# Performance work log

Hardware: AMD Instinct MI355X
Metric: run time of the kernel (lower is better)

Reference implementation:

```python
import jax, jax.numpy as jnp
import numpy as np

N = 100000
E = 1600000
D_IN, D_HID, D_OUT = 128, 32, 32
NEG_SLOPE = 0.2
EPS = 1e-16


def setup_inputs() -> dict:
    key = jax.random.key(0)
    ks = jax.random.split(key, 9)
    x = jax.random.normal(ks[0], (N, D_IN), dtype=jnp.float32)
    edge_index = jax.random.randint(ks[1], (2, E), 0, N, dtype=jnp.int64)
    W1 = jax.random.normal(ks[2], (D_IN, D_HID), dtype=jnp.float32) / np.sqrt(D_IN)
    b1 = jnp.zeros((D_HID,), dtype=jnp.float32)
    W2 = jax.random.normal(ks[3], (D_HID, D_OUT), dtype=jnp.float32) / np.sqrt(D_HID)
    att_src = jax.random.normal(ks[4], (D_OUT,), dtype=jnp.float32) / np.sqrt(D_OUT)
    att_dst = jax.random.normal(ks[5], (D_OUT,), dtype=jnp.float32) / np.sqrt(D_OUT)
    b2 = jnp.zeros((D_OUT,), dtype=jnp.float32)
    return {"x": x, "edge_index": edge_index, "W1": W1, "b1": b1,
            "W2": W2, "att_src": att_src, "att_dst": att_dst, "b2": b2}


def _add_self_loops(edge_index, n):
    loop = jnp.arange(n, dtype=edge_index.dtype)
    src = jnp.concatenate([edge_index[0], loop])
    dst = jnp.concatenate([edge_index[1], loop])
    return src, dst


def _gcn_conv(x, src, dst, W, b, n):
    # symmetric normalization with self-loops already included
    deg = jax.ops.segment_sum(jnp.ones_like(dst, dtype=x.dtype), dst, num_segments=n)
    dis = jnp.where(deg > 0, jax.lax.rsqrt(jnp.maximum(deg, 1.0)), 0.0)
    h = x @ W                               # [N, H]
    norm = dis[src] * dis[dst]              # [E2]
    msg = norm[:, None] * h[src]            # [E2, H]
    return jax.ops.segment_sum(msg, dst, num_segments=n) + b


def _gat_conv(x, src, dst, W, att_src, att_dst, b, n):
    g = x @ W                               # [N, H]
    a_s = g @ att_src                       # [N]
    a_d = g @ att_dst                       # [N]
    e = a_s[src] + a_d[dst]                 # [E2]
    e = jnp.where(e > 0, e, NEG_SLOPE * e)  # leaky_relu(0.2)
    # segment softmax over edges grouped by destination node
    emax = jax.ops.segment_max(e, dst, num_segments=n)
    ee = jnp.exp(e - emax[dst])
    esum = jax.ops.segment_sum(ee, dst, num_segments=n)
    alpha = ee / (esum[dst] + EPS)
    msg = alpha[:, None] * g[src]           # [E2, H]
    return jax.ops.segment_sum(msg, dst, num_segments=n) + b


def reference(x, edge_index, W1, b1, W2, att_src, att_dst, b2):
    n = x.shape[0]
    src, dst = _add_self_loops(edge_index, n)
    h = _gcn_conv(x, src, dst, W1, b1, n)
    h = jax.nn.relu(h)
    out = _gat_conv(h, src, dst, W2, att_src, att_dst, b2, n)
    return out
```

## Files before the change

### kernel.cpp

```cpp
#include <hip/hip_runtime.h>
#include <cstdint>
#include <cstddef>

#define D_IN   128
#define D_HID  32
#define D_OUT  32
#define NEG_SLOPE 0.2f
#define EPS_F  1e-16f

#define BKT_SHIFT 9
#define NPB (1 << BKT_SHIFT)
#define KBUKMAX 256
#define NBLK_BIN 512
#define AGG_BLOCKS 2048

using half4 = __attribute__((ext_vector_type(4))) _Float16;

__global__ void detect_kernel(const int* __restrict__ ei, long long E, int* __restrict__ flag) {
    const int t = threadIdx.x;
    long long n = E < 64 ? E : 64;
    int bad = (t < n && ei[2 * t + 1] != 0) ? 1 : 0;
    unsigned long long mask = __ballot(bad);
    if (t == 0) *flag = (mask == 0ULL) ? 1 : 0;
}

__device__ __forceinline__ int edge_val(const int* __restrict__ ei, long long idx, int is64) {
    return is64 ? ei[idx * 2] : ei[idx];
}

__global__ __launch_bounds__(256) void hist_kernel(
        const int* __restrict__ ei, const int* __restrict__ flag,
        long long E, long long E2, int* __restrict__ hist, int K2, int EPB) {
    __shared__ int hcnt[KBUKMAX];
    const int is64 = *flag;
    const int t = threadIdx.x;
    if (t < K2) hcnt[t] = 0;
    __syncthreads();
    const long long lo = (long long)blockIdx.x * EPB;
    const long long hi = min(E2, lo + EPB);
    for (long long e = lo + t; e < hi; e += 256) {
        int d = (e < E) ? edge_val(ei, E + e, is64) : (int)(e - E);
        atomicAdd(&hcnt[d >> BKT_SHIFT], 1);
    }
    __syncthreads();
    if (t < K2) hist[t * gridDim.x + blockIdx.x] = hcnt[t];
}

__global__ void scan_ga_kernel(int* __restrict__ a, int* __restrict__ bsum, int L) {
    __shared__ int wsum[4];
    const int t = threadIdx.x;
    const int i0 = blockIdx.x * 1024 + t * 4;
    int v[4]; int s = 0;
    #pragma unroll
    for (int k = 0; k < 4; ++k) {
        v[k] = (i0 + k < L) ? a[i0 + k] : 0;
        s += v[k];
    }
    const int lane = t & 63, wid = t >> 6;
    int incl = s;
    #pragma unroll
    for (int d = 1; d < 64; d <<= 1) {
        int u = __shfl_up(incl, d);
        if (lane >= d) incl += u;
    }
    if (lane == 63) wsum[wid] = incl;
    __syncthreads();
    int woff = 0;
    for (int w = 0; w < wid; ++w) woff += wsum[w];
    int excl = woff + incl - s;
    #pragma unroll
    for (int k = 0; k < 4; ++k) {
        if (i0 + k < L) a[i0 + k] = excl;
        excl += v[k];
    }
    if (t == 255) bsum[blockIdx.x] = woff + incl;
}

__global__ __launch_bounds__(1024) void scan_flat_kernel(int* __restrict__ a, int L) {
    __shared__ int wsum[16];
    __shared__ int carry_s;
    const int t = threadIdx.x;
    const int lane = t & 63, wid = t >> 6;
    if (t == 0) carry_s = 0;
    __syncthreads();
    for (int start = 0; start < L; start += 1024) {
        int idx = start + t;
        int v = (idx < L) ? a[idx] : 0;
        int incl = v;
        #pragma unroll
        for (int d = 1; d < 64; d <<= 1) {
            int u = __shfl_up(incl, d);
            if (lane >= d) incl += u;
        }
        if (lane == 63) wsum[wid] = incl;
        __syncthreads();
        int woff = 0;
        for (int w = 0; w < wid; ++w) woff += wsum[w];
        int carry = carry_s;
        __syncthreads();
        if (idx < L) a[idx] = carry + woff + incl - v;
        if (t == 1023) carry_s = carry + woff + incl;
        __syncthreads();
    }
}

__global__ void scan_gc_kernel(int* __restrict__ a, const int* __restrict__ bsum, int L) {
    int idx = blockIdx.x * blockDim.x + threadIdx.x;
    if (idx < L) a[idx] += bsum[idx >> 10];
}

__global__ __launch_bounds__(256) void scatter_kernel(
        const int* __restrict__ ei, const int* __restrict__ flag,
        long long E, long long E2, const int* __restrict__ off,
        unsigned* __restrict__ bins, int K2, int EPB) {
    __shared__ int cur[KBUKMAX];
    const int is64 = *flag;
    const int t = threadIdx.x;
    if (t < K2) cur[t] = off[t * gridDim.x + blockIdx.x];
    __syncthreads();
    const long long lo = (long long)blockIdx.x * EPB;
    const long long hi = min(E2, lo + EPB);
    for (long long e = lo + t; e < hi; e += 256) {
        int s, d;
        if (e < E) { s = edge_val(ei, e, is64); d = edge_val(ei, E + e, is64); }
        else       { s = d = (int)(e - E); }
        int b = d >> BKT_SHIFT;
        int pos = atomicAdd(&cur[b], 1);
        bins[pos] = (unsigned)s | ((unsigned)(d & (NPB - 1)) << 17);
    }
}

__global__ __launch_bounds__(512) void csr_b_kernel(
        const unsigned* __restrict__ bins, const int* __restrict__ off,
        int* __restrict__ rowptr, float* __restrict__ dis, int* __restrict__ csr_src,
        int N, int K2, long long E2) {
    __shared__ int lcur[NPB];
    __shared__ int wsum[8];
    const int b = blockIdx.x, t = threadIdx.x;
    const int nbase = b << BKT_SHIFT;
    const int nn = min(NPB, N - nbase);
    lcur[t] = 0;
    __syncthreads();
    const int base = off[b * NBLK_BIN];
    const int end  = (b == K2 - 1) ? (int)E2 : off[(b + 1) * NBLK_BIN];
    for (int i = base + t; i < end; i += 512)
        atomicAdd(&lcur[bins[i] >> 17], 1);
    __syncthreads();
    const int lane = t & 63, wid = t >> 6;
    int v = lcur[t];
    int incl = v;
    #pragma unroll
    for (int d = 1; d < 64; d <<= 1) {
        int u = __shfl_up(incl, d);
        if (lane >= d) incl += u;
    }
    if (lane == 63) wsum[wid] = incl;
    __syncthreads();
    int woff = 0;
    for (int w = 0; w < wid; ++w) woff += wsum[w];
    int excl = woff + incl - v;
    if (t < nn) {
        rowptr[nbase + t] = base + excl;
        dis[nbase + t] = rsqrtf((float)v);
    }
    __syncthreads();
    lcur[t] = base + excl;
    __syncthreads();
    for (int i = base + t; i < end; i += 512) {
        unsigned u = bins[i];
        int pos = atomicAdd(&lcur[u >> 17], 1);
        csr_src[pos] = (int)(u & 0x1FFFFu);
    }
    if (b == 0 && t == 0) rowptr[N] = (int)E2;
}

__global__ __launch_bounds__(256) void gemm1_kernel(
        const float* __restrict__ x, const float* __restrict__ W1,
        const float* __restrict__ dis, _Float16* __restrict__ hws_h, int N) {
    __shared__ float sW[D_IN * D_HID];
    const int t = threadIdx.x;
    for (int i = t; i < D_IN * D_HID; i += 256) sW[i] = W1[i];
    __syncthreads();
    long long row = (long long)blockIdx.x * 256 + t;
    const bool valid = row < N;
    long long r = valid ? row : (long long)(N - 1);
    const float4* x4 = (const float4*)x;
    float acc[D_HID];
    #pragma unroll
    for (int c = 0; c < D_HID; ++c) acc[c] = 0.f;
    for (int q = 0; q < 32; ++q) {
        float4 xv = x4[r * 32 + q];
        #pragma unroll
        for (int kk = 0; kk < 4; ++kk) {
            float xs = (&xv.x)[kk];
            const float* wrow = &sW[(q * 4 + kk) * D_HID];
            #pragma unroll
            for (int c4 = 0; c4 < 8; ++c4) {
                float4 wv = *(const float4*)&wrow[c4 * 4];
                acc[c4 * 4 + 0] = fmaf(xs, wv.x, acc[c4 * 4 + 0]);
                acc[c4 * 4 + 1] = fmaf(xs, wv.y, acc[c4 * 4 + 1]);
                acc[c4 * 4 + 2] = fmaf(xs, wv.z, acc[c4 * 4 + 2]);
                acc[c4 * 4 + 3] = fmaf(xs, wv.w, acc[c4 * 4 + 3]);
            }
        }
    }
    if (valid) {
        float dd = dis[r];
        half4* hh4 = (half4*)hws_h;
        #pragma unroll
        for (int c4 = 0; c4 < 8; ++c4) {
            half4 o;
            o.x = (_Float16)(acc[c4 * 4 + 0] * dd);
            o.y = (_Float16)(acc[c4 * 4 + 1] * dd);
            o.z = (_Float16)(acc[c4 * 4 + 2] * dd);
            o.w = (_Float16)(acc[c4 * 4 + 3] * dd);
            hh4[r * 8 + c4] = o;
        }
    }
}

__global__ void gcn_agg_kernel(const int* __restrict__ rowptr, const int* __restrict__ csr_src,
                               const _Float16* __restrict__ hws_h, const float* __restrict__ dis,
                               const float* __restrict__ b1, float* __restrict__ h1, int N) {
    const int lane = threadIdx.x & 63;
    const int u = lane & 7, grp = lane >> 3;
    const int wib = threadIdx.x >> 6;
    const half4* hh4 = (const half4*)hws_h;
    float4* h14 = (float4*)h1;
    const float4 b14 = ((const float4*)b1)[u];
    for (int i = blockIdx.x * 4 + wib; i < N; i += gridDim.x * 4) {
        const int b = rowptr[i], e = rowptr[i + 1];
        float ax = 0.f, ay = 0.f, az = 0.f, aw = 0.f;
        for (int j = b + grp; j < e; j += 8) {
            int s = csr_src[j];
            half4 hv = hh4[s * 8 + u];
            ax += (float)hv.x; ay += (float)hv.y;
            az += (float)hv.z; aw += (float)hv.w;
        }
        #pragma unroll
        for (int d = 8; d <= 32; d <<= 1) {
            ax += __shfl_xor(ax, d); ay += __shfl_xor(ay, d);
            az += __shfl_xor(az, d); aw += __shfl_xor(aw, d);
        }
        if (grp == 0) {
            float dd = dis[i];
            float4 o;
            o.x = fmaf(dd, ax, b14.x); o.y = fmaf(dd, ay, b14.y);
            o.z = fmaf(dd, az, b14.z); o.w = fmaf(dd, aw, b14.w);
            o.x = o.x > 0.f ? o.x : 0.f; o.y = o.y > 0.f ? o.y : 0.f;
            o.z = o.z > 0.f ? o.z : 0.f; o.w = o.w > 0.f ? o.w : 0.f;
            h14[(long long)i * 8 + u] = o;
        }
    }
}

__global__ void gemm2_kernel(const float* __restrict__ h1, const float* __restrict__ W2,
                             const float* __restrict__ att_s, const float* __restrict__ att_d,
                             _Float16* __restrict__ g_h, float* __restrict__ a_s,
                             float* __restrict__ a_d, int N) {
    __shared__ float sW[D_HID * D_OUT];
    __shared__ float sas[D_OUT], sad[D_OUT];
    __shared__ float sh[8][D_HID];
    const int t = threadIdx.x;
    const int c = t & 31, r = t >> 5;
    for (int i = t; i < D_HID * D_OUT; i += 256) sW[i] = W2[i];
    if (t < D_OUT) { sas[t] = att_s[t]; sad[t] = att_d[t]; }
    for (long long base = (long long)blockIdx.x * 8; base < N; base += (long long)gridDim.x * 8) {
        __syncthreads();
        if (base * D_HID + t < (long long)N * D_HID) sh[r][c] = h1[base * D_HID + t];
        __syncthreads();
        long long row = base + r;
        if (row < N) {
            float gv = 0.0f;
            #pragma unroll
            for (int k = 0; k < D_HID; ++k) gv = fmaf(sh[r][k], sW[k * D_OUT + c], gv);
            g_h[row * D_OUT + c] = (_Float16)gv;
            float ps = gv * sas[c];
            float pd = gv * sad[c];
            #pragma unroll
            for (int d = 16; d >= 1; d >>= 1) {
                ps += __shfl_xor(ps, d);
                pd += __shfl_xor(pd, d);
            }
            if (c == 0) { a_s[row] = ps; a_d[row] = pd; }
        }
    }
}

__global__ __launch_bounds__(256) void e_pre_kernel(
        const int* __restrict__ rowptr, const int* __restrict__ csr_src,
        const float* __restrict__ a_s, const float* __restrict__ a_d,
        float* __restrict__ epre, float* __restrict__ mrow, int N) {
    int i = blockIdx.x * blockDim.x + threadIdx.x;
    if (i >= N) return;
    const int b = rowptr[i], e = rowptr[i + 1];
    const float adi = a_d[i];
    float m = -1e30f;
    for (int j = b; j < e; ++j) {
        float ev = a_s[csr_src[j]] + adi;
        ev = ev > 0.f ? ev : NEG_SLOPE * ev;
        epre[j] = ev;
        m = fmaxf(m, ev);
    }
    mrow[i] = m;
}

__global__ void gat_agg_kernel(const int* __restrict__ rowptr, const int* __restrict__ csr_src,
                               const _Float16* __restrict__ g_h, const float* __restrict__ epre,
                               const float* __restrict__ mrow, const float* __restrict__ b2,
                               float* __restrict__ out, int N) {
    const int lane = threadIdx.x & 63;
    const int u = lane & 7, grp = lane >> 3;
    const int wib = threadIdx.x >> 6;
    const half4* gh4 = (const half4*)g_h;
    float4* out4 = (float4*)out;
    const float4 b24 = ((const float4*)b2)[u];
    for (int i = blockIdx.x * 4 + wib; i < N; i += gridDim.x * 4) {
        const int b = rowptr[i], e = rowptr[i + 1];
        const float mi = mrow[i];
        float ssum = 0.f;
        float ax = 0.f, ay = 0.f, az = 0.f, aw = 0.f;
        for (int j = b + grp; j < e; j += 8) {
            int s = csr_src[j];
            float w = __expf(epre[j] - mi);
            half4 gv = gh4[s * 8 + u];
            ssum += w;
            ax = fmaf(w, (float)gv.x, ax);
            ay = fmaf(w, (float)gv.y, ay);
            az = fmaf(w, (float)gv.z, az);
            aw = fmaf(w, (float)gv.w, aw);
        }
        #pragma unroll
        for (int d = 8; d <= 32; d <<= 1) {
            ssum += __shfl_xor(ssum, d);
            ax += __shfl_xor(ax, d); ay += __shfl_xor(ay, d);
            az += __shfl_xor(az, d); aw += __shfl_xor(aw, d);
        }
        if (grp == 0) {
            float inv = 1.f / (ssum + EPS_F);
            float4 o;
            o.x = fmaf(ax, inv, b24.x); o.y = fmaf(ay, inv, b24.y);
            o.z = fmaf(az, inv, b24.z); o.w = fmaf(aw, inv, b24.w);
            out4[(long long)i * 8 + u] = o;
        }
    }
}

extern "C" void kernel_launch(void* const* d_in, const int* in_sizes, int n_in,
                              void* d_out, int out_size, void* d_ws, size_t ws_size,
                              hipStream_t stream) {
    const float* x       = (const float*)d_in[0];
    const int*   ei      = (const int*)d_in[1];
    const float* W1      = (const float*)d_in[2];
    const float* b1      = (const float*)d_in[3];
    const float* W2      = (const float*)d_in[4];
    const float* att_src = (const float*)d_in[5];
    const float* att_dst = (const float*)d_in[6];
    const float* b2      = (const float*)d_in[7];
    float* out = (float*)d_out;

    const long long N  = in_sizes[0] / D_IN;
    const long long E  = in_sizes[1] / 2;
    const long long E2 = E + N;
    const int K2  = (int)((N + NPB - 1) >> BKT_SHIFT);
    const int EPB = (int)((E2 + NBLK_BIN - 1) / NBLK_BIN);
    const int LH  = K2 * NBLK_BIN;
    const int NBH = (LH + 1023) / 1024;

    char* ws = (char*)d_ws;
    size_t off0 = 0;
    auto alloc = [&](size_t bytes) -> void* {
        off0 = (off0 + 255) & ~(size_t)255;
        void* p = ws + off0;
        off0 += bytes;
        return p;
    };
    int*   flag     = (int*)  alloc(16);
    int*   hist     = (int*)  alloc((size_t)KBUKMAX * NBLK_BIN * 4);
    unsigned* bins  = (unsigned*)alloc((size_t)E2 * 4);
    int*   rowptr   = (int*)  alloc((size_t)(N + 1) * 4);
    int*   csr_src  = (int*)  alloc((size_t)E2 * 4);
    float* dis      = (float*)alloc((size_t)N * 4);
    _Float16* hws_h = (_Float16*)alloc((size_t)N * D_HID * 2);
    float* h1       = (float*)alloc((size_t)N * D_HID * 4);
    _Float16* g_h   = (_Float16*)alloc((size_t)N * D_OUT * 2);
    float* as       = (float*)alloc((size_t)N * 4);
    float* ad       = (float*)alloc((size_t)N * 4);
    float* epre     = (float*)alloc((size_t)E2 * 4);
    float* mrow     = (float*)alloc((size_t)N * 4);
    int*   bsum     = (int*)  alloc((size_t)NBH * 4);
    (void)ws_size; (void)n_in; (void)out_size;

    detect_kernel<<<1, 64, 0, stream>>>(ei, E, flag);
    hist_kernel<<<NBLK_BIN, 256, 0, stream>>>(ei, flag, E, E2, hist, K2, EPB);
    scan_ga_kernel<<<NBH, 256, 0, stream>>>(hist, bsum, LH);
    scan_flat_kernel<<<1, 1024, 0, stream>>>(bsum, NBH);
    scan_gc_kernel<<<(LH + 255) / 256, 256, 0, stream>>>(hist, bsum, LH);
    scatter_kernel<<<NBLK_BIN, 256, 0, stream>>>(ei, flag, E, E2, hist, bins, K2, EPB);
    csr_b_kernel<<<K2, 512, 0, stream>>>(bins, hist, rowptr, dis, csr_src, (int)N, K2, E2);
    gemm1_kernel<<<(int)((N + 255) / 256), 256, 0, stream>>>(x, W1, dis, hws_h, (int)N);
    gcn_agg_kernel<<<AGG_BLOCKS, 256, 0, stream>>>(rowptr, csr_src, hws_h, dis, b1, h1, (int)N);
    gemm2_kernel<<<1024, 256, 0, stream>>>(h1, W2, att_src, att_dst, g_h, as, ad, (int)N);
    e_pre_kernel<<<(int)((N + 255) / 256), 256, 0, stream>>>(rowptr, csr_src, as, ad, epre, mrow, (int)N);
    gat_agg_kernel<<<AGG_BLOCKS, 256, 0, stream>>>(rowptr, csr_src, g_h, epre, mrow, b2, out, (int)N);
}
```

Before: 189.2 us.

## Fold dtype detection and scan fixup into consumers; split waves across two rows

Removes the separate int64-detection kernel by having every hist and scatter block detect the index width itself. It also drops the scan add-back kernel by adding the block sums on the fly in scatter and csr_b. The GCN and GAT aggregation kernels now let each 64-lane wave handle two destination rows, with 32 lanes each. This is meant to cut idle lanes on rows of about 17 edges and shorten the shuffle reduction. It costs redundant detection loads in every block and a few extra bsum reads.

```diff
diff --git a/kernel.cpp b/kernel.cpp
--- a/kernel.cpp
+++ b/kernel.cpp
@@ -16,26 +16,30 @@
 
 using half4 = __attribute__((ext_vector_type(4))) _Float16;
 
-__global__ void detect_kernel(const int* __restrict__ ei, long long E, int* __restrict__ flag) {
-    const int t = threadIdx.x;
-    long long n = E < 64 ? E : 64;
-    int bad = (t < n && ei[2 * t + 1] != 0) ? 1 : 0;
-    unsigned long long mask = __ballot(bad);
-    if (t == 0) *flag = (mask == 0ULL) ? 1 : 0;
-}
-
 __device__ __forceinline__ int edge_val(const int* __restrict__ ei, long long idx, int is64) {
     return is64 ? ei[idx * 2] : ei[idx];
 }
 
+__device__ __forceinline__ int detect_is64(const int* __restrict__ ei, long long E,
+                                           int t, int* s_is64) {
+    if (t < 64) {
+        long long n = E < 64 ? E : 64;
+        int bad = (t < n && ei[2 * t + 1] != 0) ? 1 : 0;
+        unsigned long long mask = __ballot(bad);
+        if (t == 0) *s_is64 = (mask == 0ULL) ? 1 : 0;
+    }
+    __syncthreads();
+    return *s_is64;
+}
+
 __global__ __launch_bounds__(256) void hist_kernel(
-        const int* __restrict__ ei, const int* __restrict__ flag,
-        long long E, long long E2, int* __restrict__ hist, int K2, int EPB) {
+        const int* __restrict__ ei, long long E, long long E2,
+        int* __restrict__ hist, int K2, int EPB) {
     __shared__ int hcnt[KBUKMAX];
-    const int is64 = *flag;
+    __shared__ int s_is64;
     const int t = threadIdx.x;
     if (t < K2) hcnt[t] = 0;
-    __syncthreads();
+    const int is64 = detect_is64(ei, E, t, &s_is64);
     const long long lo = (long long)blockIdx.x * EPB;
     const long long hi = min(E2, lo + EPB);
     for (long long e = lo + t; e < hi; e += 256) {
@@ -104,20 +108,18 @@
     }
 }
 
-__global__ void scan_gc_kernel(int* __restrict__ a, const int* __restrict__ bsum, int L) {
-    int idx = blockIdx.x * blockDim.x + threadIdx.x;
-    if (idx < L) a[idx] += bsum[idx >> 10];
-}
-
 __global__ __launch_bounds__(256) void scatter_kernel(
-        const int* __restrict__ ei, const int* __restrict__ flag,
-        long long E, long long E2, const int* __restrict__ off,
+        const int* __restrict__ ei, long long E, long long E2,
+        const int* __restrict__ off, const int* __restrict__ bsum,
         unsigned* __restrict__ bins, int K2, int EPB) {
     __shared__ int cur[KBUKMAX];
-    const int is64 = *flag;
-    const int t = threadIdx.x;
-    if (t < K2) cur[t] = off[t * gridDim.x + blockIdx.x];
-    __syncthreads();
+    __shared__ int s_is64;
+    const int t = threadIdx.x;
+    if (t < K2) {
+        int idx = t * gridDim.x + blockIdx.x;
+        cur[t] = off[idx] + bsum[idx >> 10];
+    }
+    const int is64 = detect_is64(ei, E, t, &s_is64);
     const long long lo = (long long)blockIdx.x * EPB;
     const long long hi = min(E2, lo + EPB);
     for (long long e = lo + t; e < hi; e += 256) {
@@ -132,6 +134,7 @@
 
 __global__ __launch_bounds__(512) void csr_b_kernel(
         const unsigned* __restrict__ bins, const int* __restrict__ off,
+        const int* __restrict__ bsum,
         int* __restrict__ rowptr, float* __restrict__ dis, int* __restrict__ csr_src,
         int N, int K2, long long E2) {
     __shared__ int lcur[NPB];
@@ -141,8 +144,14 @@
     const int nn = min(NPB, N - nbase);
     lcur[t] = 0;
     __syncthreads();
-    const int base = off[b * NBLK_BIN];
-    const int end  = (b == K2 - 1) ? (int)E2 : off[(b + 1) * NBLK_BIN];
+    int bidx = b * NBLK_BIN;
+    const int base = off[bidx] + bsum[bidx >> 10];
+    int end;
+    if (b == K2 - 1) end = (int)E2;
+    else {
+        int eidx = (b + 1) * NBLK_BIN;
+        end = off[eidx] + bsum[eidx >> 10];
+    }
     for (int i = base + t; i < end; i += 512)
         atomicAdd(&lcur[bins[i] >> 17], 1);
     __syncthreads();
@@ -223,26 +232,31 @@
                                const _Float16* __restrict__ hws_h, const float* __restrict__ dis,
                                const float* __restrict__ b1, float* __restrict__ h1, int N) {
     const int lane = threadIdx.x & 63;
-    const int u = lane & 7, grp = lane >> 3;
+    const int half = lane >> 5, l32 = lane & 31;
+    const int u = l32 & 7, grp = l32 >> 3;
     const int wib = threadIdx.x >> 6;
     const half4* hh4 = (const half4*)hws_h;
     float4* h14 = (float4*)h1;
     const float4 b14 = ((const float4*)b1)[u];
-    for (int i = blockIdx.x * 4 + wib; i < N; i += gridDim.x * 4) {
-        const int b = rowptr[i], e = rowptr[i + 1];
+    const int npair = (N + 1) >> 1;
+    for (int p = blockIdx.x * 4 + wib; p < npair; p += gridDim.x * 4) {
+        const int i = p * 2 + half;
+        const bool act = i < N;
+        int b = 0, e = 0;
+        if (act) { b = rowptr[i]; e = rowptr[i + 1]; }
         float ax = 0.f, ay = 0.f, az = 0.f, aw = 0.f;
-        for (int j = b + grp; j < e; j += 8) {
+        for (int j = b + grp; j < e; j += 4) {
             int s = csr_src[j];
             half4 hv = hh4[s * 8 + u];
             ax += (float)hv.x; ay += (float)hv.y;
             az += (float)hv.z; aw += (float)hv.w;
         }
         #pragma unroll
-        for (int d = 8; d <= 32; d <<= 1) {
+        for (int d = 8; d <= 16; d <<= 1) {
             ax += __shfl_xor(ax, d); ay += __shfl_xor(ay, d);
             az += __shfl_xor(az, d); aw += __shfl_xor(aw, d);
         }
-        if (grp == 0) {
+        if (act && grp == 0) {
             float dd = dis[i];
             float4 o;
             o.x = fmaf(dd, ax, b14.x); o.y = fmaf(dd, ay, b14.y);
@@ -310,17 +324,22 @@
                                const float* __restrict__ mrow, const float* __restrict__ b2,
                                float* __restrict__ out, int N) {
     const int lane = threadIdx.x & 63;
-    const int u = lane & 7, grp = lane >> 3;
+    const int half = lane >> 5, l32 = lane & 31;
+    const int u = l32 & 7, grp = l32 >> 3;
     const int wib = threadIdx.x >> 6;
     const half4* gh4 = (const half4*)g_h;
     float4* out4 = (float4*)out;
     const float4 b24 = ((const float4*)b2)[u];
-    for (int i = blockIdx.x * 4 + wib; i < N; i += gridDim.x * 4) {
-        const int b = rowptr[i], e = rowptr[i + 1];
-        const float mi = mrow[i];
+    const int npair = (N + 1) >> 1;
+    for (int p = blockIdx.x * 4 + wib; p < npair; p += gridDim.x * 4) {
+        const int i = p * 2 + half;
+        const bool act = i < N;
+        int b = 0, e = 0;
+        float mi = 0.f;
+        if (act) { b = rowptr[i]; e = rowptr[i + 1]; mi = mrow[i]; }
         float ssum = 0.f;
         float ax = 0.f, ay = 0.f, az = 0.f, aw = 0.f;
-        for (int j = b + grp; j < e; j += 8) {
+        for (int j = b + grp; j < e; j += 4) {
             int s = csr_src[j];
             float w = __expf(epre[j] - mi);
             half4 gv = gh4[s * 8 + u];
@@ -331,12 +350,12 @@
             aw = fmaf(w, (float)gv.w, aw);
         }
         #pragma unroll
-        for (int d = 8; d <= 32; d <<= 1) {
+        for (int d = 8; d <= 16; d <<= 1) {
             ssum += __shfl_xor(ssum, d);
             ax += __shfl_xor(ax, d); ay += __shfl_xor(ay, d);
             az += __shfl_xor(az, d); aw += __shfl_xor(aw, d);
         }
-        if (grp == 0) {
+        if (act && grp == 0) {
             float inv = 1.f / (ssum + EPS_F);
             float4 o;
             o.x = fmaf(ax, inv, b24.x); o.y = fmaf(ay, inv, b24.y);
@@ -375,7 +394,6 @@
         off0 += bytes;
         return p;
     };
-    int*   flag     = (int*)  alloc(16);
     int*   hist     = (int*)  alloc((size_t)KBUKMAX * NBLK_BIN * 4);
     unsigned* bins  = (unsigned*)alloc((size_t)E2 * 4);
     int*   rowptr   = (int*)  alloc((size_t)(N + 1) * 4);
@@ -391,13 +409,11 @@
     int*   bsum     = (int*)  alloc((size_t)NBH * 4);
     (void)ws_size; (void)n_in; (void)out_size;
 
-    detect_kernel<<<1, 64, 0, stream>>>(ei, E, flag);
-    hist_kernel<<<NBLK_BIN, 256, 0, stream>>>(ei, flag, E, E2, hist, K2, EPB);
+    hist_kernel<<<NBLK_BIN, 256, 0, stream>>>(ei, E, E2, hist, K2, EPB);
     scan_ga_kernel<<<NBH, 256, 0, stream>>>(hist, bsum, LH);
     scan_flat_kernel<<<1, 1024, 0, stream>>>(bsum, NBH);
-    scan_gc_kernel<<<(LH + 255) / 256, 256, 0, stream>>>(hist, bsum, LH);
-    scatter_kernel<<<NBLK_BIN, 256, 0, stream>>>(ei, flag, E, E2, hist, bins, K2, EPB);
-    csr_b_kernel<<<K2, 512, 0, stream>>>(bins, hist, rowptr, dis, csr_src, (int)N, K2, E2);
+    scatter_kernel<<<NBLK_BIN, 256, 0, stream>>>(ei, E, E2, hist, bsum, bins, K2, EPB);
+    csr_b_kernel<<<K2, 512, 0, stream>>>(bins, hist, bsum, rowptr, dis, csr_src, (int)N, K2, E2);
     gemm1_kernel<<<(int)((N + 255) / 256), 256, 0, stream>>>(x, W1, dis, hws_h, (int)N);
     gcn_agg_kernel<<<AGG_BLOCKS, 256, 0, stream>>>(rowptr, csr_src, hws_h, dis, b1, h1, (int)N);
     gemm2_kernel<<<1024, 256, 0, stream>>>(h1, W2, att_src, att_dst, g_h, as, ad, (int)N);
```

Result: faster. 180.8 us (-4.4%).
